# Performance work log

Hardware: AMD Instinct MI355X
Metric: run time of the kernel (lower is better)

Reference implementation:

```python
import jax, jax.numpy as jnp
import numpy as np

B, S, DIM = 2, 2048, 2048
N_HEADS, N_KV_HEADS = 16, 4
HEAD_DIM = DIM // N_HEADS  # 128
N_REP = N_HEADS // N_KV_HEADS  # 4


def setup_inputs() -> dict:
    key = jax.random.key(0)
    ks = jax.random.split(key, 7)
    x = jax.random.normal(ks[0], (B, S, DIM), dtype=jnp.float32)
    cos = jax.random.uniform(ks[1], (S, HEAD_DIM // 2), dtype=jnp.float32)
    sin = jax.random.uniform(ks[2], (S, HEAD_DIM // 2), dtype=jnp.float32)
    sc = 1.0 / np.sqrt(DIM)
    wq = jax.random.normal(ks[3], (DIM, N_HEADS * HEAD_DIM), dtype=jnp.float32) * sc
    wk = jax.random.normal(ks[4], (DIM, N_KV_HEADS * HEAD_DIM), dtype=jnp.float32) * sc
    wv = jax.random.normal(ks[5], (DIM, N_KV_HEADS * HEAD_DIM), dtype=jnp.float32) * sc
    wo = jax.random.normal(ks[6], (N_HEADS * HEAD_DIM, DIM), dtype=jnp.float32) * sc
    return {"x": x, "cos": cos, "sin": sin, "wq": wq, "wk": wk, "wv": wv, "wo": wo}


def _rope(t, cos, sin):
    # t: [B, S, H, hd]; cos/sin: [S, hd/2] -> broadcast as [1, S, 1, hd/2]
    tr, ti = t[..., ::2], t[..., 1::2]
    c = cos[None, :, None, :]
    s = sin[None, :, None, :]
    out_r = tr * c - ti * s
    out_i = tr * s + ti * c
    # interleave back: stack on new last axis then flatten
    return jnp.stack([out_r, out_i], axis=-1).reshape(t.shape)


def reference(x, cos, sin, wq, wk, wv, wo):
    bsz, seqlen, _ = x.shape
    xq = (x @ wq).reshape(bsz, seqlen, N_HEADS, HEAD_DIM)
    xk = (x @ wk).reshape(bsz, seqlen, N_KV_HEADS, HEAD_DIM)
    xv = (x @ wv).reshape(bsz, seqlen, N_KV_HEADS, HEAD_DIM)
    xq = _rope(xq, cos, sin)
    xk = _rope(xk, cos, sin)
    # GQA: repeat kv heads -> [B, S, H, hd]
    xk = jnp.repeat(xk, N_REP, axis=2)
    xv = jnp.repeat(xv, N_REP, axis=2)
    scale = 1.0 / jnp.sqrt(jnp.asarray(HEAD_DIM, dtype=x.dtype))
    scores = jnp.einsum("bqhd,bkhd->bhqk", xq, xk) * scale
    causal = jnp.tril(jnp.ones((seqlen, seqlen), dtype=bool))
    scores = jnp.where(causal[None, None, :, :], scores, jnp.asarray(-jnp.inf, dtype=scores.dtype))
    attn = jax.nn.softmax(scores, axis=-1)
    out = jnp.einsum("bhqk,bkhd->bqhd", attn, xv)
    out = out.reshape(bsz, seqlen, N_HEADS * HEAD_DIM)
    return out @ wo
```

## Files before the change

kernel.cpp:

```cpp
#include <hip/hip_runtime.h>
#include <stdint.h>

#define SEQ 2048

typedef uint16_t u16;
typedef uint32_t u32;
typedef __attribute__((ext_vector_type(4))) float f32x4;
typedef __attribute__((ext_vector_type(8))) __bf16 bf16x8;
typedef __attribute__((ext_vector_type(4))) __bf16 bf16x4;

__device__ __forceinline__ u16 f2bf(float f) {
    u32 u = __float_as_uint(f);
    u += 0x7FFFu + ((u >> 16) & 1u);
    return (u16)(u >> 16);
}
__device__ __forceinline__ float bf2f(u16 h) {
    return __uint_as_float(((u32)h) << 16);
}
__device__ __forceinline__ u32 cvt_pk_bf16(float lo, float hi) {
    u32 r;
    asm("v_cvt_pk_bf16_f32 %0, %1, %2" : "=v"(r) : "v"(lo), "v"(hi));
    return r;
}
__device__ __forceinline__ void async16(const void* g, void* l) {
    auto gp = (__attribute__((address_space(1))) void*)const_cast<void*>(g);
    auto lp = (__attribute__((address_space(3))) void*)l;
    __builtin_amdgcn_global_load_lds(gp, lp, 16, 0, 0);
}

__global__ __launch_bounds__(256) void convert_bf16(const float* __restrict__ src,
                                                    u16* __restrict__ dst) {
    int i = blockIdx.x * 256 + threadIdx.x;
    float4 v = ((const float4*)src)[i];
    ((uint2*)dst)[i] = make_uint2(cvt_pk_bf16(v.x, v.y), cvt_pk_bf16(v.z, v.w));
}

__global__ __launch_bounds__(256) void tconv_all(const float* __restrict__ wq,
                                                 const float* __restrict__ wk,
                                                 const float* __restrict__ wv,
                                                 const float* __restrict__ wo,
                                                 u16* __restrict__ wqkvT,
                                                 u16* __restrict__ woT) {
    __shared__ float tile[64][65];
    const int bx = blockIdx.x, k0 = blockIdx.y * 64;
    const float* src; u16* dst; int N, n0;
    if (bx < 32)      { src = wq; dst = wqkvT;                        N = 2048; n0 = bx * 64; }
    else if (bx < 40) { src = wk; dst = wqkvT + (size_t)2048 * 2048;  N = 512;  n0 = (bx - 32) * 64; }
    else if (bx < 48) { src = wv; dst = wqkvT + (size_t)2560 * 2048;  N = 512;  n0 = (bx - 40) * 64; }
    else              { src = wo; dst = woT;                          N = 2048; n0 = (bx - 48) * 64; }
    const int tid = threadIdx.x;
#pragma unroll
    for (int p = 0; p < 4; p++) {
        int r = p * 16 + (tid >> 4);
        int c = (tid & 15) * 4;
        float4 v = *(const float4*)&src[(size_t)(k0 + r) * N + n0 + c];
        tile[r][c] = v.x; tile[r][c+1] = v.y; tile[r][c+2] = v.z; tile[r][c+3] = v.w;
    }
    __syncthreads();
#pragma unroll
    for (int p = 0; p < 4; p++) {
        int n = p * 16 + (tid >> 4);
        int kq = (tid & 15) * 4;
        u32 lo = cvt_pk_bf16(tile[kq+0][n], tile[kq+1][n]);
        u32 hi = cvt_pk_bf16(tile[kq+2][n], tile[kq+3][n]);
        *(uint2*)&dst[(size_t)(n0 + n) * 2048 + k0 + kq] = make_uint2(lo, hi);
    }
}

template <int BN, bool F32OUT>
__global__ __launch_bounds__(512, 2) void gemm256(const u16* __restrict__ A,
                                                  const u16* __restrict__ Bt,
                                                  void* __restrict__ Cv,
                                                  int N, int K, int nbx,
                                                  const float* __restrict__ cosp,
                                                  const float* __restrict__ sinp,
                                                  u16* __restrict__ vt) {
    constexpr int MF = (BN == 256) ? 8 : 4;
    constexpr int SLOT = 8192 + BN * 32;
    __shared__ u16 lds[4 * SLOT];

    const int nwg = gridDim.x;
    const int q = nwg >> 3, r = nwg & 7;
    const int xcd = blockIdx.x & 7, lid = blockIdx.x >> 3;
    const int wg = (xcd < r ? xcd * (q + 1) : r * (q + 1) + (xcd - r) * q) + lid;
    const int by = wg / nbx, bx = wg - by * nbx;
    const int m0 = by * 256, n0 = bx * BN;

    const int tid = threadIdx.x;
    const int w = tid >> 6, l = tid & 63;
    const int lr = l & 15, quad = l >> 4;
    const int wm = (BN == 256) ? (w >> 2) * 128 : (w >> 1) * 64;
    const int wn = (BN == 256) ? (w & 3) * 64  : (w & 1) * 64;
    const int cs = (quad ^ (lr & 3)) * 8;

    const int rA = w * 32 + (l >> 2);
    const int gA = ((l & 3) ^ (rA & 3)) * 8;
    const u16* aS = A + (size_t)(m0 + rA) * K + gA;
    u16* ldA = lds + (w * 128 + l) * 8;

    const u16* bS;
    u16* ldB;
    if constexpr (BN == 256) {
        bS = Bt + (size_t)(n0 + rA) * K + gA;
        ldB = lds + 8192 + (w * 128 + l) * 8;
    } else {
        const int rB = w * 16 + (l >> 2);
        const int gB = ((l & 3) ^ (rB & 3)) * 8;
        bS = Bt + (size_t)(n0 + rB) * K + gB;
        ldB = lds + 8192 + tid * 8;
    }

    f32x4 acc[MF][4] = {};
    const int nK = K >> 5;

    auto stageA = [&](int kt) {
        u16* d = ldA + (kt & 3) * SLOT;
        const u16* s = aS + (size_t)kt * 32;
        async16(s, d);
        async16(s + (size_t)16 * K, d + 512);
    };
    auto stageB = [&](int kt) {
        u16* d = ldB + (kt & 3) * SLOT;
        const u16* s = bS + (size_t)kt * 32;
        async16(s, d);
        if constexpr (BN == 256) async16(s + (size_t)16 * K, d + 512);
    };

    stageA(0); stageB(0); stageA(1); stageB(1); stageA(2); stageB(2);
    if constexpr (BN == 256)
        asm volatile("s_waitcnt vmcnt(8)" ::: "memory");
    else
        asm volatile("s_waitcnt vmcnt(6)" ::: "memory");
    __builtin_amdgcn_s_barrier();

    for (int kt = 0; kt < nK; ++kt) {
        const u16* As = lds + (kt & 3) * SLOT;
        const u16* Bs = As + 8192;
        const bool pre = (kt + 3 < nK);
        if constexpr (BN == 256) {
            bf16x8 af[4], bfr[4];
#pragma unroll
            for (int i = 0; i < 4; i++)
                af[i] = *(const bf16x8*)&As[(wm + i * 16 + lr) * 32 + cs];
#pragma unroll
            for (int i = 0; i < 4; i++)
                bfr[i] = *(const bf16x8*)&Bs[(wn + i * 16 + lr) * 32 + cs];
            if (pre) stageA(kt + 3);
            __builtin_amdgcn_s_barrier();
            asm volatile("s_waitcnt lgkmcnt(0)" ::: "memory");
            __builtin_amdgcn_s_setprio(1);
#pragma unroll
            for (int mf = 0; mf < 4; mf++)
#pragma unroll
                for (int nf = 0; nf < 4; nf++)
                    acc[mf][nf] = __builtin_amdgcn_mfma_f32_16x16x32_bf16(af[mf], bfr[nf], acc[mf][nf], 0, 0, 0);
            __builtin_amdgcn_s_setprio(0);
            __builtin_amdgcn_s_barrier();
#pragma unroll
            for (int i = 0; i < 4; i++)
                af[i] = *(const bf16x8*)&As[(wm + 64 + i * 16 + lr) * 32 + cs];
            if (pre) stageB(kt + 3);
            __builtin_amdgcn_s_barrier();
            asm volatile("s_waitcnt lgkmcnt(0)" ::: "memory");
            __builtin_amdgcn_s_setprio(1);
#pragma unroll
            for (int mf = 0; mf < 4; mf++)
#pragma unroll
                for (int nf = 0; nf < 4; nf++)
                    acc[4 + mf][nf] = __builtin_amdgcn_mfma_f32_16x16x32_bf16(af[mf], bfr[nf], acc[4 + mf][nf], 0, 0, 0);
            __builtin_amdgcn_s_setprio(0);
            if (kt < nK - 3)       asm volatile("s_waitcnt vmcnt(8)" ::: "memory");
            else if (kt == nK - 3) asm volatile("s_waitcnt vmcnt(4)" ::: "memory");
            else if (kt == nK - 2) asm volatile("s_waitcnt vmcnt(0)" ::: "memory");
            if (kt < nK - 1) __builtin_amdgcn_s_barrier();
        } else {
            bf16x8 af[MF], bfr[4];
#pragma unroll
            for (int i = 0; i < MF; i++)
                af[i] = *(const bf16x8*)&As[(wm + i * 16 + lr) * 32 + cs];
#pragma unroll
            for (int i = 0; i < 4; i++)
                bfr[i] = *(const bf16x8*)&Bs[(wn + i * 16 + lr) * 32 + cs];
            if (pre) { stageA(kt + 3); stageB(kt + 3); }
            __builtin_amdgcn_s_barrier();
            asm volatile("s_waitcnt lgkmcnt(0)" ::: "memory");
            __builtin_amdgcn_s_setprio(1);
#pragma unroll
            for (int mf = 0; mf < MF; mf++)
#pragma unroll
                for (int nf = 0; nf < 4; nf++)
                    acc[mf][nf] = __builtin_amdgcn_mfma_f32_16x16x32_bf16(af[mf], bfr[nf], acc[mf][nf], 0, 0, 0);
            __builtin_amdgcn_s_setprio(0);
            if (kt < nK - 3)       asm volatile("s_waitcnt vmcnt(6)" ::: "memory");
            else if (kt == nK - 3) asm volatile("s_waitcnt vmcnt(3)" ::: "memory");
            else if (kt == nK - 2) asm volatile("s_waitcnt vmcnt(0)" ::: "memory");
            if (kt < nK - 1) __builtin_amdgcn_s_barrier();
        }
    }

    if constexpr (BN == 256 && !F32OUT) {
        if (n0 >= 2560) {
            const int bb = m0 >> 11;
#pragma unroll
            for (int mf = 0; mf < MF; mf++) {
                const int token0 = (m0 + wm + mf * 16 + quad * 4) & (SEQ - 1);
#pragma unroll
                for (int nf = 0; nf < 4; nf++) {
                    int dg = n0 - 2560 + wn + nf * 16 + lr;
                    int kh = dg >> 7, d = dg & 127;
                    u32 lo = cvt_pk_bf16(acc[mf][nf][0], acc[mf][nf][1]);
                    u32 hi = cvt_pk_bf16(acc[mf][nf][2], acc[mf][nf][3]);
                    *(uint2*)&vt[((size_t)((bb * 4 + kh) * 128 + d)) * SEQ + token0] = make_uint2(lo, hi);
                }
            }
        } else if (n0 >= 2048) {
            const float sgn = (lr & 1) ? 1.0f : -1.0f;
#pragma unroll
            for (int mf = 0; mf < MF; mf++) {
#pragma unroll
                for (int nf = 0; nf < 4; nf++) {
                    int col = n0 + wn + nf * 16 + lr;
                    int ci = (col & 127) >> 1;
#pragma unroll
                    for (int rr = 0; rr < 4; rr++) {
                        size_t row = (size_t)(m0 + wm + mf * 16 + quad * 4 + rr);
                        int token = (int)row & (SEQ - 1);
                        float v = acc[mf][nf][rr];
                        float ppart = __shfl_xor(v, 1);
                        float c = cosp[token * 64 + ci];
                        float s = sinp[token * 64 + ci];
                        float ov = fmaf(sgn * ppart, s, v * c);
                        ((u16*)Cv)[row * (size_t)N + col] = f2bf(ov);
                    }
                }
            }
        } else {
#pragma unroll
            for (int mf = 0; mf < MF; mf++)
#pragma unroll
                for (int nf = 0; nf < 4; nf++)
#pragma unroll
                    for (int rr = 0; rr < 4; rr++) {
                        size_t row = (size_t)(m0 + wm + mf * 16 + quad * 4 + rr);
                        size_t col = (size_t)(n0 + wn + nf * 16 + lr);
                        ((u16*)Cv)[row * (size_t)N + col] = f2bf(acc[mf][nf][rr]);
                    }
        }
    } else {
#pragma unroll
        for (int mf = 0; mf < MF; mf++)
#pragma unroll
            for (int nf = 0; nf < 4; nf++)
#pragma unroll
                for (int rr = 0; rr < 4; rr++) {
                    size_t row = (size_t)(m0 + wm + mf * 16 + quad * 4 + rr);
                    size_t col = (size_t)(n0 + wn + nf * 16 + lr);
                    if (F32OUT)
                        ((float*)Cv)[row * (size_t)N + col] = acc[mf][nf][rr];
                    else
                        ((u16*)Cv)[row * (size_t)N + col] = f2bf(acc[mf][nf][rr]);
                }
    }
}

__global__ __launch_bounds__(512, 2) void flash_attn(const u16* __restrict__ qkv,
                                                     const u16* __restrict__ vt,
                                                     const float* __restrict__ cosp,
                                                     const float* __restrict__ sinp,
                                                     u16* __restrict__ ob) {
    __shared__ u16 sh[65536];
    const int bidx = blockIdx.x;
    const int xcd   = bidx & 7;
    const int inner = bidx >> 3;
    const int b  = xcd >> 2, kh = xcd & 3;
    const int h  = kh * 4 + (inner & 3);
    const int a  = inner >> 2;
    const int tid = threadIdx.x;
    const int w = tid >> 6, lane = tid & 63;
    const int grp = w >> 2, wl = w & 3;
    const int lr = lane & 15, quad = lane >> 4;
    const float qscale = 0.088388347762f * 1.4426950408889634f;

    u16* base_g = sh + grp * 24576;
    u16* vb  = base_g + 16384;
    u16* lPw = sh + 49152 + w * 2048;

    const int tidg = tid & 255;
    const int krow = tidg >> 4;
    const int kchunk = (tidg & 15) ^ krow;
    const int vrow = tidg >> 3;
    const int vchunk = (tidg & 7) ^ (vrow & 7);
    const u16* kRow = qkv + (size_t)b * SEQ * 3072 + 2048 + kh * 128
                    + (size_t)krow * 3072 + kchunk * 8;
    const u16* vRow = vt + (size_t)(b * 4 + kh) * 128 * SEQ
                    + (size_t)vrow * SEQ + vchunk * 8;

    auto stageK = [&](int kt, int buf) {
        u16* d = base_g + buf * 8192 + tidg * 8;
#pragma unroll
        for (int i = 0; i < 4; i++)
            async16(kRow + (size_t)(kt * 64 + i * 16) * 3072, d + i * 2048);
    };
    auto stageV = [&](int kt) {
        u16* d = vb + tidg * 8;
#pragma unroll
        for (int i = 0; i < 4; i++)
            async16(vRow + (size_t)(i * 32) * SEQ + kt * 64, d + i * 2048);
    };

    float* mO = (float*)sh;
    float* mM = (float*)(sh + 49152);

    for (int p = 0; p < 2; p++) {
        const int qt = p ? (7 - a) : (8 + a);
        const int niters = p ? (8 - a) : (9 + a);
        const int kt0 = grp * niters;

        stageK(kt0, 0);

        bf16x8 qf[2][4];
#pragma unroll
        for (int qi = 0; qi < 2; qi++) {
            const int token = qt * 128 + wl * 32 + qi * 16 + lr;
            const u16* qb = qkv + (size_t)(b * SEQ + token) * 3072 + h * 128;
#pragma unroll
            for (int kk = 0; kk < 4; kk++) {
                uint4 raw = *(const uint4*)(qb + kk * 32 + quad * 8);
                u32 rw[4] = {raw.x, raw.y, raw.z, raw.w};
                union { u32 u[4]; bf16x8 v; } fr;
#pragma unroll
                for (int pp = 0; pp < 4; pp++) {
                    int ci = kk * 16 + quad * 4 + pp;
                    float cv = cosp[token * 64 + ci];
                    float sv = sinp[token * 64 + ci];
                    float tr = bf2f((u16)(rw[pp] & 0xFFFFu));
                    float ti = bf2f((u16)(rw[pp] >> 16));
                    fr.u[pp] = cvt_pk_bf16((tr * cv - ti * sv) * qscale,
                                           (tr * sv + ti * cv) * qscale);
                }
                qf[qi][kk] = fr.v;
            }
        }

        f32x4 o[2][8] = {};
        float m_st[2] = {-1e30f, -1e30f};
        float l_st[2] = {0.f, 0.f};
        const int qg = qt * 128 + wl * 32 + lr;

        for (int t = 0; t < niters; t++) {
            const int kt = kt0 + t;
            const int buf = t & 1;
            stageV(kt);
            if (t + 1 < niters) {
                stageK(kt + 1, buf ^ 1);
                asm volatile("s_waitcnt vmcnt(8)" ::: "memory");
            } else {
                asm volatile("s_waitcnt vmcnt(4)" ::: "memory");
            }
            asm volatile("s_barrier" ::: "memory");

            const u16* kcur = base_g + buf * 8192;
            f32x4 sc[2][4] = {};
            __builtin_amdgcn_s_setprio(1);
#pragma unroll
            for (int nf = 0; nf < 4; nf++) {
#pragma unroll
                for (int kk = 0; kk < 4; kk++) {
                    bf16x8 ak = *(const bf16x8*)&kcur[(nf * 16 + lr) * 128 + (((kk * 4 + quad) ^ lr) * 8)];
                    sc[0][nf] = __builtin_amdgcn_mfma_f32_16x16x32_bf16(ak, qf[0][kk], sc[0][nf], 0, 0, 0);
                    sc[1][nf] = __builtin_amdgcn_mfma_f32_16x16x32_bf16(ak, qf[1][kk], sc[1][nf], 0, 0, 0);
                }
            }
            __builtin_amdgcn_s_setprio(0);

            const int kb = kt * 64 + quad * 4;
            const int kmax = kt * 64 + 63;
#pragma unroll
            for (int qi = 0; qi < 2; qi++) {
                float ps[4][4];
                float tm[4];
                const int qrow_g = qg + qi * 16;
                if (kmax > qt * 128 + wl * 32 + qi * 16) {
#pragma unroll
                    for (int nf = 0; nf < 4; nf++) {
                        tm[nf] = -1e30f;
#pragma unroll
                        for (int r = 0; r < 4; r++) {
                            float v = sc[qi][nf][r];
                            if ((kb + nf * 16 + r) > qrow_g) v = -1e30f;
                            ps[nf][r] = v;
                            tm[nf] = fmaxf(tm[nf], v);
                        }
                    }
                } else {
#pragma unroll
                    for (int nf = 0; nf < 4; nf++) {
                        tm[nf] = -1e30f;
#pragma unroll
                        for (int r = 0; r < 4; r++) {
                            float v = sc[qi][nf][r];
                            ps[nf][r] = v;
                            tm[nf] = fmaxf(tm[nf], v);
                        }
                    }
                }
                float tmax = fmaxf(fmaxf(tm[0], tm[1]), fmaxf(tm[2], tm[3]));
                tmax = fmaxf(tmax, __shfl_xor(tmax, 16));
                tmax = fmaxf(tmax, __shfl_xor(tmax, 32));
                const float mprev = m_st[qi];
                if (!__all(tmax - mprev <= 8.0f)) {
                    float mnew = fmaxf(mprev, tmax);
                    float alpha = exp2f(mprev - mnew);
                    l_st[qi] *= alpha;
                    m_st[qi] = mnew;
#pragma unroll
                    for (int r = 0; r < 4; r++) {
                        float ar = __shfl(alpha, quad * 4 + r, 16);
#pragma unroll
                        for (int nd = 0; nd < 8; nd++) o[qi][nd][r] *= ar;
                    }
                }
                const float mcur = m_st[qi];
                float rs[4];
#pragma unroll
                for (int nf = 0; nf < 4; nf++) {
                    rs[nf] = 0.f;
#pragma unroll
                    for (int r = 0; r < 4; r++) {
                        float e = exp2f(ps[nf][r] - mcur);
                        ps[nf][r] = e;
                        rs[nf] += e;
                    }
                }
                float rsum = (rs[0] + rs[1]) + (rs[2] + rs[3]);
                rsum += __shfl_xor(rsum, 16);
                rsum += __shfl_xor(rsum, 32);
                l_st[qi] += rsum;
                const int qrow = qi * 16 + lr;
#pragma unroll
                for (int nf = 0; nf < 4; nf++) {
                    u32 lo = cvt_pk_bf16(ps[nf][0], ps[nf][1]);
                    u32 hi = cvt_pk_bf16(ps[nf][2], ps[nf][3]);
                    int c = (nf * 4 + quad) ^ lr;
                    *(uint2*)&lPw[qrow * 64 + c * 4] = make_uint2(lo, hi);
                }
            }

            if (t + 1 < niters) asm volatile("s_waitcnt vmcnt(4)" ::: "memory");
            else                asm volatile("s_waitcnt vmcnt(0)" ::: "memory");
            asm volatile("s_barrier" ::: "memory");

            __builtin_amdgcn_s_setprio(1);
#pragma unroll
            for (int kf = 0; kf < 2; kf++) {
                bf16x8 pa[2];
#pragma unroll
                for (int qi = 0; qi < 2; qi++) {
                    int c0 = (kf * 8 + quad * 2) ^ lr;
                    int c1 = (kf * 8 + quad * 2 + 1) ^ lr;
                    bf16x4 p0 = *(const bf16x4*)&lPw[(qi * 16 + lr) * 64 + c0 * 4];
                    bf16x4 p1 = *(const bf16x4*)&lPw[(qi * 16 + lr) * 64 + c1 * 4];
                    pa[qi] = __builtin_shufflevector(p0, p1, 0, 1, 2, 3, 4, 5, 6, 7);
                }
#pragma unroll
                for (int nd = 0; nd < 8; nd++) {
                    bf16x8 vv = *(const bf16x8*)&vb[(nd * 16 + lr) * 64 + (((kf * 4 + quad) ^ (lr & 7)) * 8)];
                    o[0][nd] = __builtin_amdgcn_mfma_f32_16x16x32_bf16(pa[0], vv, o[0][nd], 0, 0, 0);
                    o[1][nd] = __builtin_amdgcn_mfma_f32_16x16x32_bf16(pa[1], vv, o[1][nd], 0, 0, 0);
                }
            }
            __builtin_amdgcn_s_setprio(0);

            asm volatile("s_barrier" ::: "memory");
        }

        __syncthreads();
        if (grp == 1) {
#pragma unroll
            for (int qi = 0; qi < 2; qi++) {
#pragma unroll
                for (int r = 0; r < 4; r++) {
                    int row = wl * 32 + qi * 16 + quad * 4 + r;
#pragma unroll
                    for (int nd = 0; nd < 8; nd++)
                        mO[row * 128 + nd * 16 + lr] = o[qi][nd][r];
                }
                if (quad == 0) {
                    int rowl = wl * 32 + qi * 16 + lr;
                    mM[rowl * 2]     = m_st[qi];
                    mM[rowl * 2 + 1] = l_st[qi];
                }
            }
        }
        __syncthreads();
        if (grp == 0) {
#pragma unroll
            for (int qi = 0; qi < 2; qi++) {
                int rowl = wl * 32 + qi * 16 + lr;
                float m1 = mM[rowl * 2], l1 = mM[rowl * 2 + 1];
                float M  = fmaxf(m_st[qi], m1);
                float a0 = exp2f(m_st[qi] - M);
                float a1 = exp2f(m1 - M);
                float li = 1.0f / (l_st[qi] * a0 + l1 * a1);
                u16* obase = ob + (size_t)(b * SEQ + qt * 128 + wl * 32 + qi * 16) * 2048 + h * 128;
#pragma unroll
                for (int r = 0; r < 4; r++) {
                    float a0b = __shfl(a0, quad * 4 + r, 16);
                    float a1b = __shfl(a1, quad * 4 + r, 16);
                    float lib = __shfl(li, quad * 4 + r, 16);
                    int row = wl * 32 + qi * 16 + quad * 4 + r;
#pragma unroll
                    for (int nd = 0; nd < 8; nd++) {
                        float val = (o[qi][nd][r] * a0b + mO[row * 128 + nd * 16 + lr] * a1b) * lib;
                        obase[(quad * 4 + r) * 2048 + nd * 16 + lr] = f2bf(val);
                    }
                }
            }
        }
        __syncthreads();
    }
}

extern "C" void kernel_launch(void* const* d_in, const int* in_sizes, int n_in,
                              void* d_out, int out_size, void* d_ws, size_t ws_size,
                              hipStream_t stream) {
    (void)in_sizes; (void)n_in; (void)out_size; (void)ws_size;
    const float* x    = (const float*)d_in[0];
    const float* cosp = (const float*)d_in[1];
    const float* sinp = (const float*)d_in[2];
    const float* wq   = (const float*)d_in[3];
    const float* wk   = (const float*)d_in[4];
    const float* wv   = (const float*)d_in[5];
    const float* wo   = (const float*)d_in[6];
    float* out = (float*)d_out;

    char* ws = (char*)d_ws;
    u16* xb    = (u16*)(ws);
    u16* qkvb  = (u16*)(ws + (size_t)16 * 1024 * 1024);
    u16* wqkvT = (u16*)(ws + (size_t)40 * 1024 * 1024);
    u16* woT   = (u16*)(ws + (size_t)52 * 1024 * 1024);
    u16* vtb   = (u16*)(ws + (size_t)60 * 1024 * 1024);
    u16* ob    = xb;

    convert_bf16<<<8192, 256, 0, stream>>>(x, xb);
    tconv_all<<<dim3(80, 32), 256, 0, stream>>>(wq, wk, wv, wo, wqkvT, woT);
    gemm256<256, false><<<192, 512, 0, stream>>>(xb, wqkvT, (void*)qkvb, 3072, 2048, 12,
                                                 cosp, sinp, vtb);
    flash_attn<<<256, 512, 0, stream>>>(qkvb, vtb, cosp, sinp, ob);
    gemm256<128, true><<<256, 512, 0, stream>>>(ob, woT, (void*)out, 2048, 2048, 16,
                                                nullptr, nullptr, nullptr);
}
```

Baseline: 317.9 us.

## Replace 256-tile GEMMs with unified 128x128 tile, 256-thread GEMM kernel

Both the QKV projection and the output projection GEMMs now use a single 128x128-tile kernel with 4 waves per block. It uses a combined A/B staging routine and a new two-level XOR swizzle for LDS. This gives 768 and 512 workgroups instead of 192 and 256, so the 256 CUs fill better and wave scheduling is more even. The cost is lower data reuse per tile and more global and L2 traffic. The fused RoPE and V-transpose epilogue is kept, adapted to 4 M-fragments.

```diff
diff --git a/kernel.cpp b/kernel.cpp
--- a/kernel.cpp
+++ b/kernel.cpp
@@ -67,142 +67,86 @@
     }
 }
 
-template <int BN, bool F32OUT>
-__global__ __launch_bounds__(512, 2) void gemm256(const u16* __restrict__ A,
+template <bool FUSE>
+__global__ __launch_bounds__(256, 2) void gemm128(const u16* __restrict__ A,
                                                   const u16* __restrict__ Bt,
                                                   void* __restrict__ Cv,
                                                   int N, int K, int nbx,
                                                   const float* __restrict__ cosp,
                                                   const float* __restrict__ sinp,
                                                   u16* __restrict__ vt) {
-    constexpr int MF = (BN == 256) ? 8 : 4;
-    constexpr int SLOT = 8192 + BN * 32;
-    __shared__ u16 lds[4 * SLOT];
+    __shared__ u16 lds[4 * 8192];
 
     const int nwg = gridDim.x;
     const int q = nwg >> 3, r = nwg & 7;
     const int xcd = blockIdx.x & 7, lid = blockIdx.x >> 3;
     const int wg = (xcd < r ? xcd * (q + 1) : r * (q + 1) + (xcd - r) * q) + lid;
     const int by = wg / nbx, bx = wg - by * nbx;
-    const int m0 = by * 256, n0 = bx * BN;
+    const int m0 = by * 128, n0 = bx * 128;
 
     const int tid = threadIdx.x;
     const int w = tid >> 6, l = tid & 63;
     const int lr = l & 15, quad = l >> 4;
-    const int wm = (BN == 256) ? (w >> 2) * 128 : (w >> 1) * 64;
-    const int wn = (BN == 256) ? (w & 3) * 64  : (w & 1) * 64;
-    const int cs = (quad ^ (lr & 3)) * 8;
-
-    const int rA = w * 32 + (l >> 2);
-    const int gA = ((l & 3) ^ (rA & 3)) * 8;
-    const u16* aS = A + (size_t)(m0 + rA) * K + gA;
-    u16* ldA = lds + (w * 128 + l) * 8;
-
-    const u16* bS;
-    u16* ldB;
-    if constexpr (BN == 256) {
-        bS = Bt + (size_t)(n0 + rA) * K + gA;
-        ldB = lds + 8192 + (w * 128 + l) * 8;
-    } else {
-        const int rB = w * 16 + (l >> 2);
-        const int gB = ((l & 3) ^ (rB & 3)) * 8;
-        bS = Bt + (size_t)(n0 + rB) * K + gB;
-        ldB = lds + 8192 + tid * 8;
+    const int wm = (w >> 1) * 64, wn = (w & 1) * 64;
+    const int cs = ((quad ^ (lr & 3) ^ ((lr >> 2) & 3)) & 3) * 8;
+
+    const int sr = tid >> 2;
+    const int sg = tid & 3;
+    const int swz = (sr ^ (sr >> 2)) & 3;
+    const u16* aS = A  + (size_t)(m0 + sr) * K + (sg ^ swz) * 8;
+    const u16* bS = Bt + (size_t)(n0 + sr) * K + (sg ^ swz) * 8;
+    u16* ldA = lds + tid * 8;
+    u16* ldB = lds + 4096 + tid * 8;
+
+    f32x4 acc[4][4] = {};
+    const int nK = K >> 5;
+
+    auto stage = [&](int kt) {
+        u16* dA = ldA + (kt & 3) * 8192;
+        u16* dB = ldB + (kt & 3) * 8192;
+        const u16* sa = aS + (size_t)kt * 32;
+        const u16* sb = bS + (size_t)kt * 32;
+        async16(sa, dA);
+        async16(sa + (size_t)64 * K, dA + 2048);
+        async16(sb, dB);
+        async16(sb + (size_t)64 * K, dB + 2048);
+    };
+
+    stage(0); stage(1); stage(2);
+    asm volatile("s_waitcnt vmcnt(8)" ::: "memory");
+    __builtin_amdgcn_s_barrier();
+
+    for (int kt = 0; kt < nK; ++kt) {
+        const u16* As = lds + (kt & 3) * 8192;
+        const u16* Bs = As + 4096;
+        bf16x8 af[4], bfr[4];
+#pragma unroll
+        for (int i = 0; i < 4; i++)
+            af[i] = *(const bf16x8*)&As[(wm + i * 16 + lr) * 32 + cs];
+#pragma unroll
+        for (int i = 0; i < 4; i++)
+            bfr[i] = *(const bf16x8*)&Bs[(wn + i * 16 + lr) * 32 + cs];
+        if (kt + 3 < nK) stage(kt + 3);
+        __builtin_amdgcn_s_barrier();
+        asm volatile("s_waitcnt lgkmcnt(0)" ::: "memory");
+        __builtin_amdgcn_s_setprio(1);
+#pragma unroll
+        for (int mf = 0; mf < 4; mf++)
+#pragma unroll
+            for (int nf = 0; nf < 4; nf++)
+                acc[mf][nf] = __builtin_amdgcn_mfma_f32_16x16x32_bf16(af[mf], bfr[nf], acc[mf][nf], 0, 0, 0);
+        __builtin_amdgcn_s_setprio(0);
+        if (kt < nK - 3)       asm volatile("s_waitcnt vmcnt(8)" ::: "memory");
+        else if (kt == nK - 3) asm volatile("s_waitcnt vmcnt(4)" ::: "memory");
+        else if (kt == nK - 2) asm volatile("s_waitcnt vmcnt(0)" ::: "memory");
+        if (kt < nK - 1) __builtin_amdgcn_s_barrier();
     }
 
-    f32x4 acc[MF][4] = {};
-    const int nK = K >> 5;
-
-    auto stageA = [&](int kt) {
-        u16* d = ldA + (kt & 3) * SLOT;
-        const u16* s = aS + (size_t)kt * 32;
-        async16(s, d);
-        async16(s + (size_t)16 * K, d + 512);
-    };
-    auto stageB = [&](int kt) {
-        u16* d = ldB + (kt & 3) * SLOT;
-        const u16* s = bS + (size_t)kt * 32;
-        async16(s, d);
-        if constexpr (BN == 256) async16(s + (size_t)16 * K, d + 512);
-    };
-
-    stageA(0); stageB(0); stageA(1); stageB(1); stageA(2); stageB(2);
-    if constexpr (BN == 256)
-        asm volatile("s_waitcnt vmcnt(8)" ::: "memory");
-    else
-        asm volatile("s_waitcnt vmcnt(6)" ::: "memory");
-    __builtin_amdgcn_s_barrier();
-
-    for (int kt = 0; kt < nK; ++kt) {
-        const u16* As = lds + (kt & 3) * SLOT;
-        const u16* Bs = As + 8192;
-        const bool pre = (kt + 3 < nK);
-        if constexpr (BN == 256) {
-            bf16x8 af[4], bfr[4];
-#pragma unroll
-            for (int i = 0; i < 4; i++)
-                af[i] = *(const bf16x8*)&As[(wm + i * 16 + lr) * 32 + cs];
-#pragma unroll
-            for (int i = 0; i < 4; i++)
-                bfr[i] = *(const bf16x8*)&Bs[(wn + i * 16 + lr) * 32 + cs];
-            if (pre) stageA(kt + 3);
-            __builtin_amdgcn_s_barrier();
-            asm volatile("s_waitcnt lgkmcnt(0)" ::: "memory");
-            __builtin_amdgcn_s_setprio(1);
-#pragma unroll
-            for (int mf = 0; mf < 4; mf++)
-#pragma unroll
-                for (int nf = 0; nf < 4; nf++)
-                    acc[mf][nf] = __builtin_amdgcn_mfma_f32_16x16x32_bf16(af[mf], bfr[nf], acc[mf][nf], 0, 0, 0);
-            __builtin_amdgcn_s_setprio(0);
-            __builtin_amdgcn_s_barrier();
-#pragma unroll
-            for (int i = 0; i < 4; i++)
-                af[i] = *(const bf16x8*)&As[(wm + 64 + i * 16 + lr) * 32 + cs];
-            if (pre) stageB(kt + 3);
-            __builtin_amdgcn_s_barrier();
-            asm volatile("s_waitcnt lgkmcnt(0)" ::: "memory");
-            __builtin_amdgcn_s_setprio(1);
-#pragma unroll
-            for (int mf = 0; mf < 4; mf++)
-#pragma unroll
-                for (int nf = 0; nf < 4; nf++)
-                    acc[4 + mf][nf] = __builtin_amdgcn_mfma_f32_16x16x32_bf16(af[mf], bfr[nf], acc[4 + mf][nf], 0, 0, 0);
-            __builtin_amdgcn_s_setprio(0);
-            if (kt < nK - 3)       asm volatile("s_waitcnt vmcnt(8)" ::: "memory");
-            else if (kt == nK - 3) asm volatile("s_waitcnt vmcnt(4)" ::: "memory");
-            else if (kt == nK - 2) asm volatile("s_waitcnt vmcnt(0)" ::: "memory");
-            if (kt < nK - 1) __builtin_amdgcn_s_barrier();
-        } else {
-            bf16x8 af[MF], bfr[4];
-#pragma unroll
-            for (int i = 0; i < MF; i++)
-                af[i] = *(const bf16x8*)&As[(wm + i * 16 + lr) * 32 + cs];
-#pragma unroll
-            for (int i = 0; i < 4; i++)
-                bfr[i] = *(const bf16x8*)&Bs[(wn + i * 16 + lr) * 32 + cs];
-            if (pre) { stageA(kt + 3); stageB(kt + 3); }
-            __builtin_amdgcn_s_barrier();
-            asm volatile("s_waitcnt lgkmcnt(0)" ::: "memory");
-            __builtin_amdgcn_s_setprio(1);
-#pragma unroll
-            for (int mf = 0; mf < MF; mf++)
-#pragma unroll
-                for (int nf = 0; nf < 4; nf++)
-                    acc[mf][nf] = __builtin_amdgcn_mfma_f32_16x16x32_bf16(af[mf], bfr[nf], acc[mf][nf], 0, 0, 0);
-            __builtin_amdgcn_s_setprio(0);
-            if (kt < nK - 3)       asm volatile("s_waitcnt vmcnt(6)" ::: "memory");
-            else if (kt == nK - 3) asm volatile("s_waitcnt vmcnt(3)" ::: "memory");
-            else if (kt == nK - 2) asm volatile("s_waitcnt vmcnt(0)" ::: "memory");
-            if (kt < nK - 1) __builtin_amdgcn_s_barrier();
-        }
-    }
-
-    if constexpr (BN == 256 && !F32OUT) {
+    if constexpr (FUSE) {
         if (n0 >= 2560) {
             const int bb = m0 >> 11;
 #pragma unroll
-            for (int mf = 0; mf < MF; mf++) {
+            for (int mf = 0; mf < 4; mf++) {
                 const int token0 = (m0 + wm + mf * 16 + quad * 4) & (SEQ - 1);
 #pragma unroll
                 for (int nf = 0; nf < 4; nf++) {
@@ -216,7 +160,7 @@
         } else if (n0 >= 2048) {
             const float sgn = (lr & 1) ? 1.0f : -1.0f;
 #pragma unroll
-            for (int mf = 0; mf < MF; mf++) {
+            for (int mf = 0; mf < 4; mf++) {
 #pragma unroll
                 for (int nf = 0; nf < 4; nf++) {
                     int col = n0 + wn + nf * 16 + lr;
@@ -236,7 +180,7 @@
             }
         } else {
 #pragma unroll
-            for (int mf = 0; mf < MF; mf++)
+            for (int mf = 0; mf < 4; mf++)
 #pragma unroll
                 for (int nf = 0; nf < 4; nf++)
 #pragma unroll
@@ -248,17 +192,14 @@
         }
     } else {
 #pragma unroll
-        for (int mf = 0; mf < MF; mf++)
+        for (int mf = 0; mf < 4; mf++)
 #pragma unroll
             for (int nf = 0; nf < 4; nf++)
 #pragma unroll
                 for (int rr = 0; rr < 4; rr++) {
                     size_t row = (size_t)(m0 + wm + mf * 16 + quad * 4 + rr);
                     size_t col = (size_t)(n0 + wn + nf * 16 + lr);
-                    if (F32OUT)
-                        ((float*)Cv)[row * (size_t)N + col] = acc[mf][nf][rr];
-                    else
-                        ((u16*)Cv)[row * (size_t)N + col] = f2bf(acc[mf][nf][rr]);
+                    ((float*)Cv)[row * (size_t)N + col] = acc[mf][nf][rr];
                 }
     }
 }
@@ -544,9 +485,9 @@
 
     convert_bf16<<<8192, 256, 0, stream>>>(x, xb);
     tconv_all<<<dim3(80, 32), 256, 0, stream>>>(wq, wk, wv, wo, wqkvT, woT);
-    gemm256<256, false><<<192, 512, 0, stream>>>(xb, wqkvT, (void*)qkvb, 3072, 2048, 12,
-                                                 cosp, sinp, vtb);
+    gemm128<true><<<768, 256, 0, stream>>>(xb, wqkvT, (void*)qkvb, 3072, 2048, 24,
+                                           cosp, sinp, vtb);
     flash_attn<<<256, 512, 0, stream>>>(qkvb, vtb, cosp, sinp, ob);
-    gemm256<128, true><<<256, 512, 0, stream>>>(ob, woT, (void*)out, 2048, 2048, 16,
-                                                nullptr, nullptr, nullptr);
-}
+    gemm128<false><<<512, 256, 0, stream>>>(ob, woT, (void*)out, 2048, 2048, 16,
+                                            nullptr, nullptr, nullptr);
+}
```

Measured after the change: 308.4 us. 3.0% less time.
